# Performance work log

Measured on AMD Instinct MI355X. Metric: run time of the kernel, lower is better.

Reference implementation:

```python
import jax, jax.numpy as jnp
import numpy as np

WIN = (2, 7, 7)
SHIFT = (1, 3, 3)
D, H, W = 8, 56, 56
C, NH = 128, 4
B = 8
N = WIN[0] * WIN[1] * WIN[2]  # 98


def _relative_position_index():
    d, h, w = np.meshgrid(np.arange(WIN[0]), np.arange(WIN[1]), np.arange(WIN[2]), indexing='ij')
    coords = np.stack([d.ravel(), h.ravel(), w.ravel()])  # (3, N)
    rel = coords[:, :, None] - coords[:, None, :]  # (3, N, N)
    rel = rel.transpose(1, 2, 0).astype(np.int64)
    rel[:, :, 0] += WIN[0] - 1
    rel[:, :, 1] += WIN[1] - 1
    rel[:, :, 2] += WIN[2] - 1
    rel[:, :, 0] *= (2 * WIN[1] - 1) * (2 * WIN[2] - 1)
    rel[:, :, 1] *= 2 * WIN[2] - 1
    return rel.sum(-1).astype(np.int32)  # (N, N)


def _shift_mask():
    img = np.zeros((1, D, H, W, 1), dtype=np.float32)
    cnt = 0
    for ds in (slice(0, -WIN[0]), slice(-WIN[0], -SHIFT[0]), slice(-SHIFT[0], None)):
        for hs in (slice(0, -WIN[1]), slice(-WIN[1], -SHIFT[1]), slice(-SHIFT[1], None)):
            for ws in (slice(0, -WIN[2]), slice(-WIN[2], -SHIFT[2]), slice(-SHIFT[2], None)):
                img[:, ds, hs, ws, :] = cnt
                cnt += 1
    m = img.reshape(1, D // WIN[0], WIN[0], H // WIN[1], WIN[1], W // WIN[2], WIN[2], 1)
    m = m.transpose(0, 1, 3, 5, 2, 4, 6, 7).reshape(-1, N)  # (nW, N)
    diff = m[:, None, :] - m[:, :, None]
    return np.where(diff != 0, np.float32(-100.0), np.float32(0.0))  # (nW, N, N)


def setup_inputs() -> dict:
    key = jax.random.key(0)
    ks = jax.random.split(key, 6)
    nW = (D // WIN[0]) * (H // WIN[1]) * (W // WIN[2])  # 256
    B_ = B * nW  # 2048
    table_size = (2 * WIN[0] - 1) * (2 * WIN[1] - 1) * (2 * WIN[2] - 1)  # 507
    return {
        'x': jax.random.normal(ks[0], (B_, N, C), dtype=jnp.float32),
        'qkv_w': jax.random.normal(ks[1], (3 * C, C), dtype=jnp.float32) * 0.02,
        'qkv_b': jax.random.normal(ks[2], (3 * C,), dtype=jnp.float32) * 0.02,
        'rpb_table': jax.random.normal(ks[3], (table_size, NH), dtype=jnp.float32) * 0.02,
        'proj_w': jax.random.normal(ks[4], (C, C), dtype=jnp.float32) * 0.02,
        'proj_b': jax.random.normal(ks[5], (C,), dtype=jnp.float32) * 0.02,
        'rel_index': jnp.asarray(_relative_position_index()),
        'mask': jnp.asarray(_shift_mask()),
    }


def reference(x, qkv_w, qkv_b, rpb_table, proj_w, proj_b, rel_index, mask):
    B_, n, c = x.shape
    hd = c // NH
    scale = hd ** -0.5
    # qkv projection -> (B_, n, 3, NH, hd)
    qkv = (x @ qkv_w.T + qkv_b).reshape(B_, n, 3, NH, hd)
    qkv = jnp.transpose(qkv, (2, 0, 3, 1, 4))  # (3, B_, NH, n, hd)
    q, k, v = qkv[0], qkv[1], qkv[2]
    attn = jnp.einsum('bhnd,bhmd->bhnm', q * scale, k)  # (B_, NH, n, n)
    # relative position bias gather
    bias = rpb_table[rel_index[:n, :n].reshape(-1)].reshape(n, n, NH)
    attn = attn + jnp.transpose(bias, (2, 0, 1))[None]
    # shift mask add
    nW = mask.shape[0]
    attn = attn.reshape(B_ // nW, nW, NH, n, n) + mask[None, :, None]
    attn = jax.nn.softmax(attn.reshape(B_, NH, n, n), axis=-1)
    out = jnp.einsum('bhnm,bhmd->bhnd', attn, v)
    out = jnp.transpose(out, (0, 2, 1, 3)).reshape(B_, n, c)
    return out @ proj_w.T + proj_b
```

## Files before the change

kernel.cpp:

```cpp
#include <hip/hip_runtime.h>
#include <math.h>
#include <stdint.h>


#define LOG2E   1.4426950408889634f
#define MASKNEG (-144.26950408889634f)

typedef __attribute__((ext_vector_type(8)))  short    bf16x8;
typedef __attribute__((ext_vector_type(4)))  float    f32x4;
typedef __attribute__((ext_vector_type(4)))  unsigned uint32x4;

__device__ __forceinline__ unsigned short cvt1(float f) {
    __bf16 h = (__bf16)f;
    return __builtin_bit_cast(unsigned short, h);
}
__device__ __forceinline__ unsigned cvt2(float lo, float hi) {
    return (unsigned)cvt1(lo) | ((unsigned)cvt1(hi) << 16);
}

__device__ __forceinline__ int tok_code(int t) {
    int pd = t / 49;
    int r  = t - pd * 49;
    int ph = r / 7;
    int pw = r - ph * 7;
    return (pd >= 1 ? 1 : 0) | (ph >= 4 ? 2 : 0) | (pw >= 4 ? 4 : 0);
}

__device__ __forceinline__ float mterm(unsigned pk, int sh, unsigned ci, unsigned cls) {
    return ((((pk >> sh) & 255u) ^ ci) & cls) ? MASKNEG : 0.f;
}

__device__ __forceinline__ int swz(int row, int col) {
    return row * 128 + (((col >> 3) ^ (row & 7)) << 3) + (col & 7);
}
__device__ __forceinline__ int vswz(int row, int col) {
    return row * 128 + ((((col >> 3) ^ (row & 7) ^ ((row >> 2) & 3)) & 15) << 3) + (col & 7);
}

template<bool BIG>
__global__ void prep_kernel(const float* __restrict__ qkv_w,
                            const float* __restrict__ proj_w,
                            const float* __restrict__ rpb_table,
                            const int*   __restrict__ rel_index,
                            unsigned short* __restrict__ wqkv,
                            unsigned short* __restrict__ wproj,
                            void* __restrict__ btab) {
    int tid = blockIdx.x * blockDim.x + threadIdx.x;
    int stride = gridDim.x * blockDim.x;
    for (int i = tid; i < 384 * 128; i += stride) wqkv[i]  = cvt1(qkv_w[i]);
    for (int i = tid; i < 128 * 128; i += stride) wproj[i] = cvt1(proj_w[i]);
    if constexpr (BIG) {
        float* bm = (float*)btab;
        for (int idx = tid; idx < 32 * 112 * 112; idx += stride) {
            int ch = idx / 12544; int r = idx - ch * 12544;
            int i  = r / 112;     int j = r - i * 112;
            int cls = ch >> 2, h = ch & 3;
            float v;
            if (i < 98) {
                if (j < 98) {
                    float bias = rpb_table[rel_index[i * 98 + j] * 4 + h];
                    bool  msk  = (((unsigned)tok_code(i) ^ (unsigned)tok_code(j)) & (unsigned)cls) != 0;
                    v = bias * LOG2E + (msk ? MASKNEG : 0.f);
                } else v = -INFINITY;
            } else v = 0.f;
            bm[idx] = v;
        }
    } else {
        unsigned short* biasL = (unsigned short*)btab;
        for (int idx = tid; idx < 4 * 112 * 112; idx += stride) {
            int h = idx / 12544; int r = idx - h * 12544;
            int i = r / 112;     int j = r - i * 112;
            float v;
            if (i < 98) v = (j < 98) ? rpb_table[rel_index[i * 98 + j] * 4 + h] * LOG2E
                                     : -INFINITY;
            else v = 0.f;
            biasL[idx] = cvt1(v);
        }
    }
}

template<bool BIG>
__global__ __launch_bounds__(1024)
void swin_main(const float* __restrict__ x,
               const float* __restrict__ qkv_b,
               const float* __restrict__ proj_b,
               const unsigned short* __restrict__ wqkv,
               const unsigned short* __restrict__ wproj,
               const void* __restrict__ btab,
               float* __restrict__ out)
{
    extern __shared__ unsigned short lds[];
    unsigned short* q_lds  = lds;
    unsigned short* k_lds  = lds + 14336;
    unsigned short* vT_lds = lds + 28672;
    unsigned short* xo_lds = lds + 45056;

    const int b    = blockIdx.x;
    const int tid  = threadIdx.x;
    const int wv   = tid >> 6;
    const int lane = tid & 63;
    const int l4   = lane >> 4;
    const int lc   = lane & 15;

    {
        int idx2 = tid * 2;
        int row  = idx2 >> 4;
        int c    = 112 + (idx2 & 15);
        *(unsigned int*)(vT_lds + vswz(row, c)) = 0u;
    }

    {
        const float* xb = x + (size_t)b * 12544;
        for (int idx = tid; idx < 3584; idx += 1024) {
            int tok = idx >> 5;
            int c   = (idx & 31) << 2;
            float4 v;
            if (tok < 98) v = *(const float4*)(xb + tok * 128 + c);
            else { v.x = 0.f; v.y = 0.f; v.z = 0.f; v.w = 0.f; }
            uint2 hv; hv.x = cvt2(v.x, v.y); hv.y = cvt2(v.z, v.w);
            *(uint2*)(xo_lds + swz(tok, c)) = hv;
        }
    }
    __syncthreads();

    {
        const int ct = wv;
        bf16x8 wf[4];
        f32x4  bias;
        const unsigned short* wrow = wqkv + (ct * 16 + lc) * 128;
#pragma unroll
        for (int kt = 0; kt < 4; ++kt) wf[kt] = *(const bf16x8*)(wrow + kt * 32 + l4 * 8);
#pragma unroll
        for (int r = 0; r < 4; ++r) bias[r] = qkv_b[ct * 16 + l4 * 4 + r];
        const bool  isq = (ct < 8);
        const float qs  = 0.17677669529663689f * LOG2E;
#pragma unroll
        for (int t = 0; t < 7; ++t) {
            bf16x8 xf[4];
#pragma unroll
            for (int kt = 0; kt < 4; ++kt)
                xf[kt] = *(bf16x8*)(xo_lds + swz(t * 16 + lc, kt * 32 + l4 * 8));
            f32x4 acc = bias;
#pragma unroll
            for (int kt = 0; kt < 4; ++kt)
                acc = __builtin_amdgcn_mfma_f32_16x16x32_bf16(wf[kt], xf[kt], acc, 0, 0, 0);
            int tok = t * 16 + lc;
            if (isq) {
                uint2 hv; hv.x = cvt2(acc[0] * qs, acc[1] * qs); hv.y = cvt2(acc[2] * qs, acc[3] * qs);
                *(uint2*)(q_lds + swz(tok, ct * 16 + l4 * 4)) = hv;
            } else {
                uint2 hv; hv.x = cvt2(acc[0], acc[1]); hv.y = cvt2(acc[2], acc[3]);
                *(uint2*)(k_lds + swz(tok, (ct - 8) * 16 + l4 * 4)) = hv;
            }
        }
        const int vd = (wv >> 1) * 16;
        bf16x8 wf2[4];
        const unsigned short* wrow2 = wqkv + (256 + vd + lc) * 128;
#pragma unroll
        for (int kt = 0; kt < 4; ++kt) wf2[kt] = *(const bf16x8*)(wrow2 + kt * 32 + l4 * 8);
        f32x4 bias2;
#pragma unroll
        for (int r = 0; r < 4; ++r) bias2[r] = qkv_b[256 + vd + l4 * 4 + r];
        const int t0 = (wv & 1) ? 4 : 0, t1 = (wv & 1) ? 7 : 4;
        for (int t = t0; t < t1; ++t) {
            bf16x8 xf[4];
#pragma unroll
            for (int kt = 0; kt < 4; ++kt)
                xf[kt] = *(bf16x8*)(xo_lds + swz(t * 16 + lc, kt * 32 + l4 * 8));
            f32x4 acc = bias2;
#pragma unroll
            for (int kt = 0; kt < 4; ++kt)
                acc = __builtin_amdgcn_mfma_f32_16x16x32_bf16(wf2[kt], xf[kt], acc, 0, 0, 0);
            int tok = t * 16 + lc;
            const int rb = vd + l4 * 4;
            vT_lds[vswz(rb + 0, tok)] = cvt1(acc[0]);
            vT_lds[vswz(rb + 1, tok)] = cvt1(acc[1]);
            vT_lds[vswz(rb + 2, tok)] = cvt1(acc[2]);
            vT_lds[vswz(rb + 3, tok)] = cvt1(acc[3]);
        }
    }
    __syncthreads();

    const int wi  = b & 255;
    const unsigned int cls =
        ((wi >> 6) == 3 ? 1u : 0u) | (((wi >> 3) & 7) == 7 ? 2u : 0u) | ((wi & 7) == 7 ? 4u : 0u);

    unsigned int jcp[7];
    if constexpr (!BIG) {
#pragma unroll
        for (int jt = 0; jt < 7; ++jt) {
            int jb = jt * 16 + l4 * 4;
            unsigned int p = 0;
#pragma unroll
            for (int r = 0; r < 4; ++r) p |= (unsigned)tok_code(jb + r < 98 ? jb + r : 0) << (8 * r);
            jcp[jt] = p;
        }
    }

    const int  srcA = ((l4 & 1) * 2) * 16 + lc;
    const int  srcB = srcA + 16;
    const bool phi  = (l4 >> 1) != 0;

    for (int pass = 0; pass < 2; ++pass) {
        int task = wv + (pass << 4);
        if (task >= 28) break;
        int h  = task / 7;
        int it = task - h * 7;
        const int i_tok = it * 16 + lc;
        const bf16x8 qfrag = *(bf16x8*)(q_lds + swz(i_tok, h * 32 + l4 * 8));

        f32x4 cvec[7];
        if constexpr (BIG) {
            const float* bmrow = (const float*)btab + ((size_t)((int)cls * 4 + h) * 112 + i_tok) * 112;
#pragma unroll
            for (int jt = 0; jt < 7; ++jt)
                cvec[jt] = *(const f32x4*)(bmrow + jt * 16 + l4 * 4);
        } else {
            const unsigned short* brow = (const unsigned short*)btab + (h * 112 + i_tok) * 112;
            const unsigned int ci = (unsigned)tok_code(i_tok < 98 ? i_tok : 0);
            ushort4 bb[7];
#pragma unroll
            for (int jt = 0; jt < 7; ++jt)
                bb[jt] = *(const ushort4*)(brow + jt * 16 + l4 * 4);
#pragma unroll
            for (int jt = 0; jt < 7; ++jt) {
                cvec[jt][0] = __builtin_bit_cast(float, (unsigned)bb[jt].x << 16) + mterm(jcp[jt], 0,  ci, cls);
                cvec[jt][1] = __builtin_bit_cast(float, (unsigned)bb[jt].y << 16) + mterm(jcp[jt], 8,  ci, cls);
                cvec[jt][2] = __builtin_bit_cast(float, (unsigned)bb[jt].z << 16) + mterm(jcp[jt], 16, ci, cls);
                cvec[jt][3] = __builtin_bit_cast(float, (unsigned)bb[jt].w << 16) + mterm(jcp[jt], 24, ci, cls);
            }
        }

        f32x4 s[7];
#pragma unroll
        for (int jt = 0; jt < 7; ++jt) {
            bf16x8 kfrag = *(bf16x8*)(k_lds + swz(jt * 16 + lc, h * 32 + l4 * 8));
            s[jt] = __builtin_amdgcn_mfma_f32_16x16x32_bf16(kfrag, qfrag, cvec[jt], 0, 0, 0);
        }

        float lsum = 0.f;
        unsigned dw[8][2];
#pragma unroll
        for (int jt = 0; jt < 7; ++jt) {
            float p0 = exp2f(s[jt][0]);
            float p1 = exp2f(s[jt][1]);
            float p2 = exp2f(s[jt][2]);
            float p3 = exp2f(s[jt][3]);
            lsum += (p0 + p1) + (p2 + p3);
            dw[jt][0] = cvt2(p0, p1);
            dw[jt][1] = cvt2(p2, p3);
        }
        dw[7][0] = 0u; dw[7][1] = 0u;

        f32x4 o0 = {0.f, 0.f, 0.f, 0.f}, o1 = {0.f, 0.f, 0.f, 0.f};
#pragma unroll
        for (int jt4 = 0; jt4 < 4; ++jt4) {
            unsigned a0 = dw[2 * jt4][0],     a1 = dw[2 * jt4][1];
            unsigned b0 = dw[2 * jt4 + 1][0], b1 = dw[2 * jt4 + 1][1];
            unsigned xA0 = __shfl((int)a0, srcA), yA0 = __shfl((int)b0, srcA);
            unsigned xA1 = __shfl((int)a1, srcA), yA1 = __shfl((int)b1, srcA);
            unsigned xB0 = __shfl((int)a0, srcB), yB0 = __shfl((int)b0, srcB);
            unsigned xB1 = __shfl((int)a1, srcB), yB1 = __shfl((int)b1, srcB);
            uint32x4 pu = { phi ? yA0 : xA0, phi ? yA1 : xA1,
                            phi ? yB0 : xB0, phi ? yB1 : xB1 };
            bf16x8 pfrag = __builtin_bit_cast(bf16x8, pu);
            bf16x8 va = *(bf16x8*)(vT_lds + vswz(h * 32 + lc,      jt4 * 32 + l4 * 8));
            bf16x8 vb = *(bf16x8*)(vT_lds + vswz(h * 32 + 16 + lc, jt4 * 32 + l4 * 8));
            o0 = __builtin_amdgcn_mfma_f32_16x16x32_bf16(va, pfrag, o0, 0, 0, 0);
            o1 = __builtin_amdgcn_mfma_f32_16x16x32_bf16(vb, pfrag, o1, 0, 0, 0);
        }
        lsum += __shfl_xor(lsum, 16);
        lsum += __shfl_xor(lsum, 32);

        float inv = 1.0f / lsum;
        uint2 h0, h1;
        h0.x = cvt2(o0[0] * inv, o0[1] * inv); h0.y = cvt2(o0[2] * inv, o0[3] * inv);
        h1.x = cvt2(o1[0] * inv, o1[1] * inv); h1.y = cvt2(o1[2] * inv, o1[3] * inv);
        *(uint2*)(xo_lds + swz(i_tok, h * 32 + l4 * 4)) = h0;
        *(uint2*)(xo_lds + swz(i_tok, h * 32 + 16 + l4 * 4)) = h1;
    }
    __syncthreads();

    {
        const int ct = wv >> 1;
        bf16x8 pw[4];
#pragma unroll
        for (int kt = 0; kt < 4; ++kt)
            pw[kt] = *(const bf16x8*)(wproj + (ct * 16 + lc) * 128 + kt * 32 + l4 * 8);
        f32x4 pbias;
#pragma unroll
        for (int r = 0; r < 4; ++r) pbias[r] = proj_b[ct * 16 + l4 * 4 + r];

        float* ob = out + (size_t)b * 12544;
        const int t0 = (wv & 1) ? 4 : 0, t1 = (wv & 1) ? 7 : 4;
        for (int t = t0; t < t1; ++t) {
            f32x4 acc = pbias;
#pragma unroll
            for (int kt = 0; kt < 4; ++kt) {
                bf16x8 of = *(bf16x8*)(xo_lds + swz(t * 16 + lc, kt * 32 + l4 * 8));
                acc = __builtin_amdgcn_mfma_f32_16x16x32_bf16(pw[kt], of, acc, 0, 0, 0);
            }
            int tok = t * 16 + lc;
            if (tok < 98) {
                float4 st; st.x = acc[0]; st.y = acc[1]; st.z = acc[2]; st.w = acc[3];
                *(float4*)(ob + tok * 128 + ct * 16 + l4 * 4) = st;
            }
        }
    }
}

extern "C" void kernel_launch(void* const* d_in, const int* in_sizes, int n_in,
                              void* d_out, int out_size, void* d_ws, size_t ws_size,
                              hipStream_t stream) {
    const float* x       = (const float*)d_in[0];
    const float* qkv_w   = (const float*)d_in[1];
    const float* qkv_b   = (const float*)d_in[2];
    const float* rpb_tab = (const float*)d_in[3];
    const float* proj_w  = (const float*)d_in[4];
    const float* proj_b  = (const float*)d_in[5];
    const int*   rel_idx = (const int*)d_in[6];

    unsigned short* wqkv  = (unsigned short*)d_ws;
    unsigned short* wproj = (unsigned short*)((char*)d_ws + 98304);
    void*           btab  = (void*)((char*)d_ws + 131072);
    float*          out   = (float*)d_out;

    const bool big = ws_size >= (size_t)(131072 + 32 * 112 * 112 * 4);
    const int LDS_BYTES = 118784;

    if (big) {
        hipLaunchKernelGGL((prep_kernel<true>), dim3(512), dim3(256), 0, stream,
                           qkv_w, proj_w, rpb_tab, rel_idx, wqkv, wproj, btab);
        (void)hipFuncSetAttribute((const void*)(swin_main<true>),
                                  hipFuncAttributeMaxDynamicSharedMemorySize, LDS_BYTES);
        hipLaunchKernelGGL((swin_main<true>), dim3(2048), dim3(1024), LDS_BYTES, stream,
                           x, qkv_b, proj_b, wqkv, wproj, btab, out);
    } else {
        hipLaunchKernelGGL((prep_kernel<false>), dim3(512), dim3(256), 0, stream,
                           qkv_w, proj_w, rpb_tab, rel_idx, wqkv, wproj, btab);
        (void)hipFuncSetAttribute((const void*)(swin_main<false>),
                                  hipFuncAttributeMaxDynamicSharedMemorySize, LDS_BYTES);
        hipLaunchKernelGGL((swin_main<false>), dim3(2048), dim3(1024), LDS_BYTES, stream,
                           x, qkv_b, proj_b, wqkv, wproj, btab, out);
    }
}
```

Measured before the change: 141.2 us.

## Shrink LDS footprint by aliasing buffers and unswizzled V^T to raise occupancy

Reorganizes shared memory: Q/K shrink to 98 rows, and the attention output reuses the Q buffer. The V^T buffer aliases the x staging buffer, so V results are held in registers until a barrier and then written to a compact unswizzled 112-stride layout. This cuts per-block LDS from about 116KB to about 77KB, aiming to fit two 1024-thread blocks per CU, and launch bounds are tightened to match. The costs are an extra barrier, possible LDS bank conflicts on the unswizzled V^T accesses, and tighter register limits.

```diff
diff --git a/kernel.cpp b/kernel.cpp
--- a/kernel.cpp
+++ b/kernel.cpp
@@ -32,9 +32,6 @@
 
 __device__ __forceinline__ int swz(int row, int col) {
     return row * 128 + (((col >> 3) ^ (row & 7)) << 3) + (col & 7);
-}
-__device__ __forceinline__ int vswz(int row, int col) {
-    return row * 128 + ((((col >> 3) ^ (row & 7) ^ ((row >> 2) & 3)) & 15) << 3) + (col & 7);
 }
 
 template<bool BIG>
@@ -80,7 +77,7 @@
 }
 
 template<bool BIG>
-__global__ __launch_bounds__(1024)
+__global__ __launch_bounds__(1024, 8)
 void swin_main(const float* __restrict__ x,
                const float* __restrict__ qkv_b,
                const float* __restrict__ proj_b,
@@ -90,10 +87,9 @@
                float* __restrict__ out)
 {
     extern __shared__ unsigned short lds[];
-    unsigned short* q_lds  = lds;
-    unsigned short* k_lds  = lds + 14336;
-    unsigned short* vT_lds = lds + 28672;
-    unsigned short* xo_lds = lds + 45056;
+    unsigned short* q_w  = lds;
+    unsigned short* k_w  = lds + 12544;
+    unsigned short* xv_w = lds + 25088;
 
     const int b    = blockIdx.x;
     const int tid  = threadIdx.x;
@@ -102,23 +98,21 @@
     const int l4   = lane >> 4;
     const int lc   = lane & 15;
 
-    {
-        int idx2 = tid * 2;
-        int row  = idx2 >> 4;
-        int c    = 112 + (idx2 & 15);
-        *(unsigned int*)(vT_lds + vswz(row, c)) = 0u;
-    }
+    if (tid < 8) *(unsigned*)(xv_w + 14336 + tid * 2) = 0u;
 
     {
         const float* xb = x + (size_t)b * 12544;
-        for (int idx = tid; idx < 3584; idx += 1024) {
+#pragma unroll
+        for (int i = 0; i < 4; ++i) {
+            int idx = tid + i * 1024;
+            if (idx >= 3584) break;
             int tok = idx >> 5;
             int c   = (idx & 31) << 2;
             float4 v;
             if (tok < 98) v = *(const float4*)(xb + tok * 128 + c);
             else { v.x = 0.f; v.y = 0.f; v.z = 0.f; v.w = 0.f; }
             uint2 hv; hv.x = cvt2(v.x, v.y); hv.y = cvt2(v.z, v.w);
-            *(uint2*)(xo_lds + swz(tok, c)) = hv;
+            *(uint2*)(xv_w + swz(tok, c)) = hv;
         }
     }
     __syncthreads();
@@ -139,21 +133,29 @@
             bf16x8 xf[4];
 #pragma unroll
             for (int kt = 0; kt < 4; ++kt)
-                xf[kt] = *(bf16x8*)(xo_lds + swz(t * 16 + lc, kt * 32 + l4 * 8));
+                xf[kt] = *(bf16x8*)(xv_w + swz(t * 16 + lc, kt * 32 + l4 * 8));
             f32x4 acc = bias;
 #pragma unroll
             for (int kt = 0; kt < 4; ++kt)
                 acc = __builtin_amdgcn_mfma_f32_16x16x32_bf16(wf[kt], xf[kt], acc, 0, 0, 0);
             int tok = t * 16 + lc;
-            if (isq) {
-                uint2 hv; hv.x = cvt2(acc[0] * qs, acc[1] * qs); hv.y = cvt2(acc[2] * qs, acc[3] * qs);
-                *(uint2*)(q_lds + swz(tok, ct * 16 + l4 * 4)) = hv;
-            } else {
-                uint2 hv; hv.x = cvt2(acc[0], acc[1]); hv.y = cvt2(acc[2], acc[3]);
-                *(uint2*)(k_lds + swz(tok, (ct - 8) * 16 + l4 * 4)) = hv;
+            if (tok < 98) {
+                if (isq) {
+                    uint2 hv; hv.x = cvt2(acc[0] * qs, acc[1] * qs); hv.y = cvt2(acc[2] * qs, acc[3] * qs);
+                    *(uint2*)(q_w + swz(tok, ct * 16 + l4 * 4)) = hv;
+                } else {
+                    uint2 hv; hv.x = cvt2(acc[0], acc[1]); hv.y = cvt2(acc[2], acc[3]);
+                    *(uint2*)(k_w + swz(tok, (ct - 8) * 16 + l4 * 4)) = hv;
+                }
             }
         }
-        const int vd = (wv >> 1) * 16;
+    }
+
+    f32x4 vacc[4];
+    const int vd = (wv >> 1) * 16;
+    const int t0 = (wv & 1) ? 4 : 0;
+    const int nt = (wv & 1) ? 3 : 4;
+    {
         bf16x8 wf2[4];
         const unsigned short* wrow2 = wqkv + (256 + vd + lc) * 128;
 #pragma unroll
@@ -161,22 +163,33 @@
         f32x4 bias2;
 #pragma unroll
         for (int r = 0; r < 4; ++r) bias2[r] = qkv_b[256 + vd + l4 * 4 + r];
-        const int t0 = (wv & 1) ? 4 : 0, t1 = (wv & 1) ? 7 : 4;
-        for (int t = t0; t < t1; ++t) {
+#pragma unroll
+        for (int ti = 0; ti < 4; ++ti) {
+            if (ti >= nt) break;
+            int t = t0 + ti;
             bf16x8 xf[4];
 #pragma unroll
             for (int kt = 0; kt < 4; ++kt)
-                xf[kt] = *(bf16x8*)(xo_lds + swz(t * 16 + lc, kt * 32 + l4 * 8));
+                xf[kt] = *(bf16x8*)(xv_w + swz(t * 16 + lc, kt * 32 + l4 * 8));
             f32x4 acc = bias2;
 #pragma unroll
             for (int kt = 0; kt < 4; ++kt)
                 acc = __builtin_amdgcn_mfma_f32_16x16x32_bf16(wf2[kt], xf[kt], acc, 0, 0, 0);
-            int tok = t * 16 + lc;
+            vacc[ti] = acc;
+        }
+    }
+    __syncthreads();
+
+    {
+#pragma unroll
+        for (int ti = 0; ti < 4; ++ti) {
+            if (ti >= nt) break;
+            int tok = (t0 + ti) * 16 + lc;
             const int rb = vd + l4 * 4;
-            vT_lds[vswz(rb + 0, tok)] = cvt1(acc[0]);
-            vT_lds[vswz(rb + 1, tok)] = cvt1(acc[1]);
-            vT_lds[vswz(rb + 2, tok)] = cvt1(acc[2]);
-            vT_lds[vswz(rb + 3, tok)] = cvt1(acc[3]);
+            xv_w[(rb + 0) * 112 + tok] = cvt1(vacc[ti][0]);
+            xv_w[(rb + 1) * 112 + tok] = cvt1(vacc[ti][1]);
+            xv_w[(rb + 2) * 112 + tok] = cvt1(vacc[ti][2]);
+            xv_w[(rb + 3) * 112 + tok] = cvt1(vacc[ti][3]);
         }
     }
     __syncthreads();
@@ -207,7 +220,7 @@
         int h  = task / 7;
         int it = task - h * 7;
         const int i_tok = it * 16 + lc;
-        const bf16x8 qfrag = *(bf16x8*)(q_lds + swz(i_tok, h * 32 + l4 * 8));
+        const bf16x8 qfrag = *(bf16x8*)(q_w + swz(i_tok, h * 32 + l4 * 8));
 
         f32x4 cvec[7];
         if constexpr (BIG) {
@@ -234,7 +247,7 @@
         f32x4 s[7];
 #pragma unroll
         for (int jt = 0; jt < 7; ++jt) {
-            bf16x8 kfrag = *(bf16x8*)(k_lds + swz(jt * 16 + lc, h * 32 + l4 * 8));
+            bf16x8 kfrag = *(bf16x8*)(k_w + swz(jt * 16 + lc, h * 32 + l4 * 8));
             s[jt] = __builtin_amdgcn_mfma_f32_16x16x32_bf16(kfrag, qfrag, cvec[jt], 0, 0, 0);
         }
 
@@ -264,8 +277,8 @@
             uint32x4 pu = { phi ? yA0 : xA0, phi ? yA1 : xA1,
                             phi ? yB0 : xB0, phi ? yB1 : xB1 };
             bf16x8 pfrag = __builtin_bit_cast(bf16x8, pu);
-            bf16x8 va = *(bf16x8*)(vT_lds + vswz(h * 32 + lc,      jt4 * 32 + l4 * 8));
-            bf16x8 vb = *(bf16x8*)(vT_lds + vswz(h * 32 + 16 + lc, jt4 * 32 + l4 * 8));
+            bf16x8 va = *(bf16x8*)(xv_w + (h * 32 + lc) * 112      + jt4 * 32 + l4 * 8);
+            bf16x8 vb = *(bf16x8*)(xv_w + (h * 32 + 16 + lc) * 112 + jt4 * 32 + l4 * 8);
             o0 = __builtin_amdgcn_mfma_f32_16x16x32_bf16(va, pfrag, o0, 0, 0, 0);
             o1 = __builtin_amdgcn_mfma_f32_16x16x32_bf16(vb, pfrag, o1, 0, 0, 0);
         }
@@ -273,11 +286,13 @@
         lsum += __shfl_xor(lsum, 32);
 
         float inv = 1.0f / lsum;
-        uint2 h0, h1;
-        h0.x = cvt2(o0[0] * inv, o0[1] * inv); h0.y = cvt2(o0[2] * inv, o0[3] * inv);
-        h1.x = cvt2(o1[0] * inv, o1[1] * inv); h1.y = cvt2(o1[2] * inv, o1[3] * inv);
-        *(uint2*)(xo_lds + swz(i_tok, h * 32 + l4 * 4)) = h0;
-        *(uint2*)(xo_lds + swz(i_tok, h * 32 + 16 + l4 * 4)) = h1;
+        if (i_tok < 98) {
+            uint2 h0, h1;
+            h0.x = cvt2(o0[0] * inv, o0[1] * inv); h0.y = cvt2(o0[2] * inv, o0[3] * inv);
+            h1.x = cvt2(o1[0] * inv, o1[1] * inv); h1.y = cvt2(o1[2] * inv, o1[3] * inv);
+            *(uint2*)(q_w + swz(i_tok, h * 32 + l4 * 4)) = h0;
+            *(uint2*)(q_w + swz(i_tok, h * 32 + 16 + l4 * 4)) = h1;
+        }
     }
     __syncthreads();
 
@@ -292,12 +307,12 @@
         for (int r = 0; r < 4; ++r) pbias[r] = proj_b[ct * 16 + l4 * 4 + r];
 
         float* ob = out + (size_t)b * 12544;
-        const int t0 = (wv & 1) ? 4 : 0, t1 = (wv & 1) ? 7 : 4;
-        for (int t = t0; t < t1; ++t) {
+        const int tt0 = (wv & 1) ? 4 : 0, tt1 = (wv & 1) ? 7 : 4;
+        for (int t = tt0; t < tt1; ++t) {
             f32x4 acc = pbias;
 #pragma unroll
             for (int kt = 0; kt < 4; ++kt) {
-                bf16x8 of = *(bf16x8*)(xo_lds + swz(t * 16 + lc, kt * 32 + l4 * 8));
+                bf16x8 of = *(bf16x8*)(q_w + swz(t * 16 + lc, kt * 32 + l4 * 8));
                 acc = __builtin_amdgcn_mfma_f32_16x16x32_bf16(pw[kt], of, acc, 0, 0, 0);
             }
             int tok = t * 16 + lc;
@@ -326,7 +341,7 @@
     float*          out   = (float*)d_out;
 
     const bool big = ws_size >= (size_t)(131072 + 32 * 112 * 112 * 4);
-    const int LDS_BYTES = 118784;
+    const int LDS_BYTES = 78880;
 
     if (big) {
         hipLaunchKernelGGL((prep_kernel<true>), dim3(512), dim3(256), 0, stream,
```

Result: faster. 124.9 us (-11.5%).
